# Optimization experiments

Measured on AMD Instinct MI355X. Metric: run time of the kernel, lower is better.

Reference implementation:

```python
import jax, jax.numpy as jnp
import numpy as np

jax.config.update("jax_enable_x64", True)

N = 100000          # occupied voxels
C = 64              # channels
K = 27              # 3x3x3 kernel volume
GRID = 80           # voxel grid extent
SHARED_FXP_SHIFT = 23
SHIFT0 = 31         # SharedFxpShift + requant_shift for input requant
SHIFT1 = 31         # SharedFxpShift + requant_shift after conv1+PReLU
PRELU_SHIFT = 25    # PReLU slope fixed-point shift (slope = round(a * 2^25))
ACT_RANGE = 127


def _build_neighbor_maps(rng):
    # sample N unique occupied voxels in an 80^3 grid
    flat = rng.choice(GRID ** 3, size=N, replace=False)
    x = flat // (GRID * GRID)
    y = (flat // GRID) % GRID
    z = flat % GRID
    G2 = GRID + 2  # pad by 1 so shifted coords stay in-range
    lut = -np.ones(G2 * G2 * G2, dtype=np.int64)
    lut[(x + 1) * G2 * G2 + (y + 1) * G2 + (z + 1)] = np.arange(N)
    offs = [(dx, dy, dz) for dx in (-1, 0, 1) for dy in (-1, 0, 1) for dz in (-1, 0, 1)]
    in_idx = np.empty((N, K), dtype=np.int64)
    for k, (dx, dy, dz) in enumerate(offs):
        in_idx[:, k] = lut[(x + dx + 1) * G2 * G2 + (y + dy + 1) * G2 + (z + dz + 1)]
    mask = in_idx >= 0
    in_idx = np.where(mask, in_idx, 0)
    return in_idx.astype(np.int32), mask


def setup_inputs() -> dict:
    rng = np.random.default_rng(0)
    in_idx, mask = _build_neighbor_maps(rng)
    x32 = rng.integers(-20000, 20000, size=(N, C)).astype(np.int32)
    w1 = rng.integers(-127, 128, size=(K, C, C)).astype(np.int8)   # [k, out, in]
    w2 = rng.integers(-127, 128, size=(K, C, C)).astype(np.int8)
    b1 = rng.integers(-1000, 1000, size=(C,)).astype(np.int32)
    b2 = rng.integers(-1000, 1000, size=(C,)).astype(np.int32)
    comp1 = rng.integers(-500, 500, size=(K, C)).astype(np.int32)  # zero-point compensation
    comp2 = rng.integers(-500, 500, size=(K, C)).astype(np.int32)
    mul1 = rng.integers(1000000, 1200000, size=(C,)).astype(np.int64)  # per-channel requant_mul (uint32 range)
    return {
        "x32": jnp.asarray(x32),
        "in_idx": jnp.asarray(in_idx),
        "mask": jnp.asarray(mask),
        "w1": jnp.asarray(w1), "b1": jnp.asarray(b1), "comp1": jnp.asarray(comp1),
        "w2": jnp.asarray(w2), "b2": jnp.asarray(b2), "comp2": jnp.asarray(comp2),
        "mul0": jnp.asarray(13675000, dtype=jnp.int64),
        "mul1": jnp.asarray(mul1),
        "slope": jnp.asarray(6710886, dtype=jnp.int64),  # round(0.2 * 2^25)
    }


def _requant_to_int8(x, mul, total_shift):
    # RequantFxpToScaledInt8: fixed-point multiply, arithmetic shift, clip to int8 range
    v = (x.astype(jnp.int64) * mul) >> total_shift
    return jnp.clip(v, -ACT_RANGE, ACT_RANGE).astype(jnp.int8)


def _sparse_conv_in8w8out32(f8, w, b, comp, in_idx, mask):
    # per-offset gather-GEMM-scatter, expressed as one masked gather + batched int8 GEMM
    g = jnp.where(mask[:, :, None], f8[in_idx], jnp.int8(0))           # [N, K, Cin] int8
    acc = jnp.einsum("nki,koi->no", g, w, preferred_element_type=jnp.int32)  # int32 accum
    # zero-point compensation added once per valid (offset, out) pair, plus bias
    acc = acc + mask.astype(jnp.int32) @ comp + b[None, :]
    return acc


def _prelu_int32(x, slope):
    x64 = x.astype(jnp.int64)
    return jnp.where(x64 >= 0, x64, (x64 * slope) >> PRELU_SHIFT)


def reference(x32, in_idx, mask, w1, b1, comp1, w2, b2, comp2, mul0, mul1, slope):
    q0 = _requant_to_int8(x32, mul0, SHIFT0)                 # int32 -> int8
    a1 = _sparse_conv_in8w8out32(q0, w1, b1, comp1, in_idx, mask)  # int32
    p1 = _prelu_int32(a1, slope)                             # int64 fixed-point PReLU
    q1 = _requant_to_int8(p1, mul1[None, :], SHIFT1)         # per-channel requant -> int8
    a2 = _sparse_conv_in8w8out32(q1, w2, b2, comp2, in_idx, mask)  # int32
    return a2 + x32                                          # int32 residual add
```

## Files before the change

### kernel.cpp

```cpp
#include <hip/hip_runtime.h>
#include <stdint.h>

#define CCH 64
#define KK 27
#define WN (KK * CCH * CCH)

typedef int v4i __attribute__((ext_vector_type(4)));

__global__ void __launch_bounds__(256) k_prep(
    const int* __restrict__ x32, const int* __restrict__ mul0p,
    const int* __restrict__ w1_32, const int* __restrict__ w2_32,
    const int* __restrict__ comp1, const int* __restrict__ b1,
    const int* __restrict__ comp2, const int* __restrict__ b2,
    const int* __restrict__ mask,
    int8_t* __restrict__ w1e, int8_t* __restrict__ w2e,
    int* __restrict__ q0, int* __restrict__ q1, int8_t* __restrict__ af,
    int pb1, int af_blocks, int nvox, int total4)
{
    const int bid = blockIdx.x;
    if (bid < pb1) {
        const int gtid = bid * 256 + threadIdx.x;
        if (gtid < WN) {
            w1e[gtid] = (int8_t)w1_32[gtid];
        } else if (gtid < 2 * WN) {
            w2e[gtid - WN] = (int8_t)w2_32[gtid - WN];
        } else if (gtid < 2 * WN + 8192) {
            int u = gtid - 2 * WN;
            const int which = u >> 12;
            u &= 4095;
            const int col = u >> 6, j = u & 63;
            const int* comp = which ? comp2 : comp1;
            const int* bias = which ? b2 : b1;
            int v;
            if (j < 27)       v = comp[j * CCH + col] >> 2;
            else if (j < 54)  v = comp[(j - 27) * CCH + col] & 3;
            else if (j == 54) v = bias[col] >> 6;
            else if (j == 55) v = bias[col] & 63;
            else              v = 0;
            (which ? w2e : w1e)[27 * 4096 + col * 64 + j] = (int8_t)v;
        } else {
            const int u = gtid - 2 * WN - 8192;
            if (u < 16)       q0[(size_t)nvox * 16 + u] = 0;
            else if (u < 32)  q1[(size_t)nvox * 16 + (u - 16)] = 0;
        }
    } else if (bid < pb1 + af_blocks) {
        const int vox = (bid - pb1) * 256 + threadIdx.x;
        if (vox < nvox) {
            int m[27];
#pragma unroll
            for (int k = 0; k < 27; ++k)
                m[k] = mask[(size_t)vox * 27 + k] ? 1 : 0;
            v4i d0, d1, d2, d3;
#pragma unroll
            for (int di = 0; di < 16; ++di) {
                int pk = 0;
#pragma unroll
                for (int b = 0; b < 4; ++b) {
                    const int ch = di * 4 + b;
                    int bv = 0;
                    if (ch < 27)       bv = m[ch] << 2;
                    else if (ch < 54)  bv = m[ch - 27];
                    else if (ch == 54) bv = 64;
                    else if (ch == 55) bv = 1;
                    pk |= bv << (8 * b);
                }
                if (di < 4)       d0[di] = pk;
                else if (di < 8)  d1[di - 4] = pk;
                else if (di < 12) d2[di - 8] = pk;
                else              d3[di - 12] = pk;
            }
            v4i* dst = (v4i*)(af + (size_t)vox * 64);
            dst[0] = d0; dst[1] = d1; dst[2] = d2; dst[3] = d3;
        }
    } else {
        const int i = (bid - pb1 - af_blocks) * 256 + threadIdx.x;
        if (i < total4) {
            const int mul2 = (*mul0p) << 1;
            const int4 v = ((const int4*)x32)[i];
            int r = 0, q;
            q = __mulhi(v.x, mul2); q = q > 127 ? 127 : (q < -127 ? -127 : q); r |= (q & 0xff);
            q = __mulhi(v.y, mul2); q = q > 127 ? 127 : (q < -127 ? -127 : q); r |= (q & 0xff) << 8;
            q = __mulhi(v.z, mul2); q = q > 127 ? 127 : (q < -127 ? -127 : q); r |= (q & 0xff) << 16;
            q = __mulhi(v.w, mul2); q = q > 127 ? 127 : (q < -127 ? -127 : q); r |= (q & 0xff) << 24;
            q0[i] = r;
        }
    }
}

template <int LAYER>
__global__ void __launch_bounds__(256, 2)
k_conv(const int8_t* __restrict__ fin,
       const int* __restrict__ in_idx,
       const int* __restrict__ mask,
       const int8_t* __restrict__ wext,
       const int8_t* __restrict__ af,
       const int* __restrict__ mul1,
       const int* __restrict__ slopep,
       const int* __restrict__ x32,
       int8_t* __restrict__ q1out,
       int* __restrict__ out,
       int nvox, int ntiles)
{
    __shared__ int s_off[2][16 * KK];
    __shared__ v4i s_red[2][4][4][64];

    const int tid  = threadIdx.x;
    const int lane = tid & 63;
    const int wv   = tid >> 6;
    const int arow = lane & 15;
    const int srow = lane >> 4;
    const int col  = wv * 16 + arow;
    const int e0 = tid;
    const int e1 = tid + 176;

    v4i wreg[7][4];
#pragma unroll
    for (int j = 0; j < 7; ++j)
#pragma unroll
        for (int g = 0; g < 4; ++g)
            wreg[j][g] = *(const v4i*)(wext +
                ((size_t)((7 * wv + j) * CCH + g * 16 + arow)) * CCH + srow * 16);

    const int mul2     = (LAYER == 1) ? (mul1[col] << 1) : 0;
    const int slope128 = (LAYER == 1) ? ((*slopep) << 7) : 0;

    const int stride = gridDim.x;
    const int t0 = blockIdx.x;
    if (t0 >= ntiles) return;
    const int cnt = (ntiles - 1 - t0) / stride + 1;

    v4i aA[7], aB[7];
    v4i accP = {0, 0, 0, 0};

#define GATHER_A(AN, SN, NB)                                                   \
    _Pragma("unroll")                                                          \
    for (int j = 0; j < 7; ++j) {                                              \
        if (wv == 3 && j == 6) {                                               \
            AN[6] = *(const v4i*)(af + (size_t)((NB) + arow) * CCH + srow * 16); \
        } else {                                                               \
            const int off_ = s_off[SN][arow * KK + (7 * wv + j)];              \
            AN[j] = *(const v4i*)(fin + off_ + srow * 16);                     \
        }                                                                      \
    }

#define EPILOGUE(TOT, NBP, X0, X1, X2, X3)                                     \
    if (LAYER == 1) {                                                          \
        int8_t* rp_ = q1out + (size_t)((NBP) + srow * 4) * CCH + col;          \
        _Pragma("unroll")                                                      \
        for (int r = 0; r < 4; ++r) {                                          \
            const int v_ = TOT[r];                                             \
            const int p_ = (v_ >= 0) ? v_ : __mulhi(v_, slope128);             \
            int q_ = __mulhi(p_, mul2);                                        \
            q_ = q_ > 127 ? 127 : (q_ < -127 ? -127 : q_);                     \
            rp_[r * CCH] = (int8_t)q_;                                         \
        }                                                                      \
    } else {                                                                   \
        int* rp_ = out + (size_t)((NBP) + srow * 4) * CCH + col;               \
        rp_[0 * CCH] = TOT[0] + X0;                                            \
        rp_[1 * CCH] = TOT[1] + X1;                                            \
        rp_[2 * CCH] = TOT[2] + X2;                                            \
        rp_[3 * CCH] = TOT[3] + X3;                                            \
    }

#define ITER(AC, AN, P, DO_EPI)                                                \
    do {                                                                       \
                      \
        int tp2_ = t + 2 * stride; if (tp2_ >= ntiles) tp2_ = ntiles - 1;      \
        const size_t b2_ = (size_t)tp2_ * (16 * KK);                           \
        const int qa0_ = in_idx[b2_ + e0], qm0_ = mask[b2_ + e0];              \
        const int qa1_ = in_idx[b2_ + e1], qm1_ = mask[b2_ + e1];              \
        const int nbp_ = (t - stride) * 16;                                    \
        int xr0_ = 0, xr1_ = 0, xr2_ = 0, xr3_ = 0;                            \
        if (DO_EPI && LAYER == 2) {                                            \
            const int* xp_ = x32 + (size_t)(nbp_ + srow * 4) * CCH + col;      \
            xr0_ = xp_[0 * CCH]; xr1_ = xp_[1 * CCH];                          \
            xr2_ = xp_[2 * CCH]; xr3_ = xp_[3 * CCH];                          \
        }                                                                      \
                                          \
        GATHER_A(AN, (P) ^ 1, (t + stride < ntiles ? (t + stride) * 16 : (ntiles - 1) * 16)) \
        __builtin_amdgcn_sched_barrier(0);                                     \
                                                       \
        v4i acc0 = {0,0,0,0}, acc1 = {0,0,0,0}, acc2 = {0,0,0,0}, acc3 = {0,0,0,0}; \
        _Pragma("unroll")                                                      \
        for (int j = 0; j < 7; ++j) {                                          \
            acc0 = __builtin_amdgcn_mfma_i32_16x16x64_i8(AC[j], wreg[j][0], acc0, 0, 0, 0); \
            acc1 = __builtin_amdgcn_mfma_i32_16x16x64_i8(AC[j], wreg[j][1], acc1, 0, 0, 0); \
            acc2 = __builtin_amdgcn_mfma_i32_16x16x64_i8(AC[j], wreg[j][2], acc2, 0, 0, 0); \
            acc3 = __builtin_amdgcn_mfma_i32_16x16x64_i8(AC[j], wreg[j][3], acc3, 0, 0, 0); \
        }                                                                      \
                      \
        if (wv != 0) s_red[P][wv][0][lane] = acc0;                             \
        if (wv != 1) s_red[P][wv][1][lane] = acc1;                             \
        if (wv != 2) s_red[P][wv][2][lane] = acc2;                             \
        if (wv != 3) s_red[P][wv][3][lane] = acc3;                             \
                       \
        if (DO_EPI) {                                                          \
            v4i tot = accP;                                                    \
            _Pragma("unroll")                                                  \
            for (int w = 0; w < 4; ++w) {                                      \
                if (w != wv) {                                                 \
                    const v4i r_ = s_red[(P) ^ 1][w][wv][lane];                \
                    tot[0] += r_[0]; tot[1] += r_[1];                          \
                    tot[2] += r_[2]; tot[3] += r_[3];                          \
                }                                                              \
            }                                                                  \
            EPILOGUE(tot, nbp_, xr0_, xr1_, xr2_, xr3_)                        \
        }                                                                      \
                         \
        s_off[P][e0] = (qm0_ ? qa0_ : nvox) << 6;                              \
        s_off[P][e1] = (qm1_ ? qa1_ : nvox) << 6;                              \
        accP = (wv == 0) ? acc0 : (wv == 1) ? acc1 : (wv == 2) ? acc2 : acc3;  \
        asm volatile("s_waitcnt lgkmcnt(0)" ::: "memory");                     \
        __builtin_amdgcn_s_barrier();                                          \
    } while (0)

    int pa0, pa1, pm0, pm1;
    {
        const size_t base = (size_t)t0 * (16 * KK);
        const int a0 = in_idx[base + e0], m0 = mask[base + e0];
        const int a1 = in_idx[base + e1], m1 = mask[base + e1];
        s_off[0][e0] = (m0 ? a0 : nvox) << 6;
        s_off[0][e1] = (m1 ? a1 : nvox) << 6;
    }
    {
        int t1c = t0 + stride; if (t1c >= ntiles) t1c = ntiles - 1;
        const size_t base = (size_t)t1c * (16 * KK);
        pa0 = in_idx[base + e0]; pm0 = mask[base + e0];
        pa1 = in_idx[base + e1]; pm1 = mask[base + e1];
    }
    __syncthreads();
    GATHER_A(aA, 0, t0 * 16)
    s_off[1][e0] = (pm0 ? pa0 : nvox) << 6;
    s_off[1][e1] = (pm1 ? pa1 : nvox) << 6;
    asm volatile("s_waitcnt lgkmcnt(0)" ::: "memory");
    __builtin_amdgcn_s_barrier();

    int t = t0;
    ITER(aA, aB, 0, 0);
    t += stride;
    int i = 1;
    while (i < cnt) {
        ITER(aB, aA, 1, 1);
        ++i; t += stride; if (i >= cnt) break;
        ITER(aA, aB, 0, 1);
        ++i; t += stride;
    }

    {
        const int pl = (cnt - 1) & 1;
        const int nbl = (t0 + (cnt - 1) * stride) * 16;
        int x0 = 0, x1 = 0, x2 = 0, x3 = 0;
        if (LAYER == 2) {
            const int* xp_ = x32 + (size_t)(nbl + srow * 4) * CCH + col;
            x0 = xp_[0 * CCH]; x1 = xp_[1 * CCH];
            x2 = xp_[2 * CCH]; x3 = xp_[3 * CCH];
        }
        v4i tot = accP;
#pragma unroll
        for (int w = 0; w < 4; ++w) {
            if (w != wv) {
                const v4i r_ = s_red[pl][w][wv][lane];
                tot[0] += r_[0]; tot[1] += r_[1];
                tot[2] += r_[2]; tot[3] += r_[3];
            }
        }
        EPILOGUE(tot, nbl, x0, x1, x2, x3)
    }
#undef ITER
#undef EPILOGUE
#undef GATHER_A
}

extern "C" void kernel_launch(void* const* d_in, const int* in_sizes, int n_in,
                              void* d_out, int out_size, void* d_ws, size_t ws_size,
                              hipStream_t stream) {
    const int* x32    = (const int*)d_in[0];
    const int* in_idx = (const int*)d_in[1];
    const int* mask   = (const int*)d_in[2];
    const int* w1_32  = (const int*)d_in[3];
    const int* b1     = (const int*)d_in[4];
    const int* comp1  = (const int*)d_in[5];
    const int* w2_32  = (const int*)d_in[6];
    const int* b2     = (const int*)d_in[7];
    const int* comp2  = (const int*)d_in[8];
    const int* mul0   = (const int*)d_in[9];
    const int* mul1   = (const int*)d_in[10];
    const int* slope  = (const int*)d_in[11];

    const int nvox = in_sizes[0] / CCH;
    const size_t wext_b = (size_t)28 * CCH * CCH;
    const size_t fbytes = (size_t)(nvox + 1) * CCH;
    const size_t falign = (fbytes + 255) & ~(size_t)255;
    const size_t walign = (wext_b + 255) & ~(size_t)255;

    int8_t* q0;
    int8_t* q1;
    int8_t* w1e;
    int8_t* w2e;
    int8_t* af;
    if (ws_size >= 3 * falign + 2 * walign) {
        q0  = (int8_t*)d_ws;
        q1  = q0 + falign;
        w1e = q1 + falign;
        w2e = w1e + walign;
        af  = w2e + walign;
    } else {
        q0  = (int8_t*)d_out;
        q1  = (int8_t*)d_ws;
        w1e = q1 + falign;
        w2e = w1e + walign;
        af  = w2e + walign;
    }

    const int total4 = (nvox * CCH) / 4;
    const int pb1 = (2 * WN + 8192 + 32 + 255) / 256;
    const int af_blocks  = (nvox + 255) / 256;
    const int req_blocks = (total4 + 255) / 256;
    k_prep<<<pb1 + af_blocks + req_blocks, 256, 0, stream>>>(
        x32, mul0, w1_32, w2_32, comp1, b1, comp2, b2, mask,
        w1e, w2e, (int*)q0, (int*)q1, af, pb1, af_blocks, nvox, total4);

    const int ntiles = nvox / 16;
    int cblocks = 512;
    if (cblocks > ntiles) cblocks = ntiles;
    k_conv<1><<<cblocks, 256, 0, stream>>>(q0, in_idx, mask, w1e, af,
                                           mul1, slope, nullptr,
                                           q1, nullptr, nvox, ntiles);
    k_conv<2><<<cblocks, 256, 0, stream>>>(q1, in_idx, mask, w2e, af,
                                           nullptr, nullptr, x32,
                                           nullptr, (int*)d_out, nvox, ntiles);
}
```

Measured before the change: 56.27 us.

## Fuse prep and both sparse conv layers into one cooperative persistent kernel

```diff
diff --git a/kernel.cpp b/kernel.cpp
--- a/kernel.cpp
+++ b/kernel.cpp
@@ -1,117 +1,46 @@
 #include <hip/hip_runtime.h>
+#include <hip/hip_cooperative_groups.h>
 #include <stdint.h>
+
+namespace cg = cooperative_groups;
 
 #define CCH 64
 #define KK 27
 #define WN (KK * CCH * CCH)
+#define WEXT (28 * CCH * CCH)
 
 typedef int v4i __attribute__((ext_vector_type(4)));
 
-__global__ void __launch_bounds__(256) k_prep(
-    const int* __restrict__ x32, const int* __restrict__ mul0p,
-    const int* __restrict__ w1_32, const int* __restrict__ w2_32,
-    const int* __restrict__ comp1, const int* __restrict__ b1,
-    const int* __restrict__ comp2, const int* __restrict__ b2,
-    const int* __restrict__ mask,
-    int8_t* __restrict__ w1e, int8_t* __restrict__ w2e,
-    int* __restrict__ q0, int* __restrict__ q1, int8_t* __restrict__ af,
-    int pb1, int af_blocks, int nvox, int total4)
+struct ConvShared {
+    int off[2][16][36];
+    v4i red[2][4][4][64];
+};
+
+template <int LAYER>
+__device__ void conv_phase(
+    ConvShared& sh,
+    const int8_t* __restrict__ fin, const int* __restrict__ in_idx,
+    const int* __restrict__ mask, const int8_t* __restrict__ wext,
+    const int8_t* __restrict__ af, const int* __restrict__ mul1,
+    const int* __restrict__ slopep, const int* __restrict__ x32,
+    int8_t* __restrict__ q1out, int* __restrict__ out,
+    int nvox, int ntiles)
 {
-    const int bid = blockIdx.x;
-    if (bid < pb1) {
-        const int gtid = bid * 256 + threadIdx.x;
-        if (gtid < WN) {
-            w1e[gtid] = (int8_t)w1_32[gtid];
-        } else if (gtid < 2 * WN) {
-            w2e[gtid - WN] = (int8_t)w2_32[gtid - WN];
-        } else if (gtid < 2 * WN + 8192) {
-            int u = gtid - 2 * WN;
-            const int which = u >> 12;
-            u &= 4095;
-            const int col = u >> 6, j = u & 63;
-            const int* comp = which ? comp2 : comp1;
-            const int* bias = which ? b2 : b1;
-            int v;
-            if (j < 27)       v = comp[j * CCH + col] >> 2;
-            else if (j < 54)  v = comp[(j - 27) * CCH + col] & 3;
-            else if (j == 54) v = bias[col] >> 6;
-            else if (j == 55) v = bias[col] & 63;
-            else              v = 0;
-            (which ? w2e : w1e)[27 * 4096 + col * 64 + j] = (int8_t)v;
-        } else {
-            const int u = gtid - 2 * WN - 8192;
-            if (u < 16)       q0[(size_t)nvox * 16 + u] = 0;
-            else if (u < 32)  q1[(size_t)nvox * 16 + (u - 16)] = 0;
-        }
-    } else if (bid < pb1 + af_blocks) {
-        const int vox = (bid - pb1) * 256 + threadIdx.x;
-        if (vox < nvox) {
-            int m[27];
-#pragma unroll
-            for (int k = 0; k < 27; ++k)
-                m[k] = mask[(size_t)vox * 27 + k] ? 1 : 0;
-            v4i d0, d1, d2, d3;
-#pragma unroll
-            for (int di = 0; di < 16; ++di) {
-                int pk = 0;
-#pragma unroll
-                for (int b = 0; b < 4; ++b) {
-                    const int ch = di * 4 + b;
-                    int bv = 0;
-                    if (ch < 27)       bv = m[ch] << 2;
-                    else if (ch < 54)  bv = m[ch - 27];
-                    else if (ch == 54) bv = 64;
-                    else if (ch == 55) bv = 1;
-                    pk |= bv << (8 * b);
-                }
-                if (di < 4)       d0[di] = pk;
-                else if (di < 8)  d1[di - 4] = pk;
-                else if (di < 12) d2[di - 8] = pk;
-                else              d3[di - 12] = pk;
-            }
-            v4i* dst = (v4i*)(af + (size_t)vox * 64);
-            dst[0] = d0; dst[1] = d1; dst[2] = d2; dst[3] = d3;
-        }
-    } else {
-        const int i = (bid - pb1 - af_blocks) * 256 + threadIdx.x;
-        if (i < total4) {
-            const int mul2 = (*mul0p) << 1;
-            const int4 v = ((const int4*)x32)[i];
-            int r = 0, q;
-            q = __mulhi(v.x, mul2); q = q > 127 ? 127 : (q < -127 ? -127 : q); r |= (q & 0xff);
-            q = __mulhi(v.y, mul2); q = q > 127 ? 127 : (q < -127 ? -127 : q); r |= (q & 0xff) << 8;
-            q = __mulhi(v.z, mul2); q = q > 127 ? 127 : (q < -127 ? -127 : q); r |= (q & 0xff) << 16;
-            q = __mulhi(v.w, mul2); q = q > 127 ? 127 : (q < -127 ? -127 : q); r |= (q & 0xff) << 24;
-            q0[i] = r;
-        }
-    }
-}
-
-template <int LAYER>
-__global__ void __launch_bounds__(256, 2)
-k_conv(const int8_t* __restrict__ fin,
-       const int* __restrict__ in_idx,
-       const int* __restrict__ mask,
-       const int8_t* __restrict__ wext,
-       const int8_t* __restrict__ af,
-       const int* __restrict__ mul1,
-       const int* __restrict__ slopep,
-       const int* __restrict__ x32,
-       int8_t* __restrict__ q1out,
-       int* __restrict__ out,
-       int nvox, int ntiles)
-{
-    __shared__ int s_off[2][16 * KK];
-    __shared__ v4i s_red[2][4][4][64];
-
     const int tid  = threadIdx.x;
     const int lane = tid & 63;
     const int wv   = tid >> 6;
     const int arow = lane & 15;
     const int srow = lane >> 4;
     const int col  = wv * 16 + arow;
+
     const int e0 = tid;
     const int e1 = tid + 176;
+    const int r0 = e0 / 27, s0 = e0 - r0 * 27;
+    const int r1 = e1 / 27, s1 = e1 - r1 * 27;
+    const int slot0 = r0 * 36 + (s0 / 7) * 8 + (s0 % 7);
+    const int slot1 = r1 * 36 + (s1 / 7) * 8 + (s1 % 7);
+    int* const offl = &sh.off[0][0][0];
+    const int OFFSTR = 16 * 36;
 
     v4i wreg[7][4];
 #pragma unroll
@@ -126,20 +55,24 @@
 
     const int stride = gridDim.x;
     const int t0 = blockIdx.x;
-    if (t0 >= ntiles) return;
     const int cnt = (ntiles - 1 - t0) / stride + 1;
 
     v4i aA[7], aB[7];
     v4i accP = {0, 0, 0, 0};
 
 #define GATHER_A(AN, SN, NB)                                                   \
-    _Pragma("unroll")                                                          \
-    for (int j = 0; j < 7; ++j) {                                              \
-        if (wv == 3 && j == 6) {                                               \
-            AN[6] = *(const v4i*)(af + (size_t)((NB) + arow) * CCH + srow * 16); \
-        } else {                                                               \
-            const int off_ = s_off[SN][arow * KK + (7 * wv + j)];              \
-            AN[j] = *(const v4i*)(fin + off_ + srow * 16);                     \
+    {                                                                          \
+        const v4i o0_ = *(const v4i*)&sh.off[SN][arow][wv * 8];                \
+        const v4i o1_ = *(const v4i*)&sh.off[SN][arow][wv * 8 + 4];            \
+        const int offs_[7] = {o0_[0], o0_[1], o0_[2], o0_[3],                  \
+                              o1_[0], o1_[1], o1_[2]};                         \
+        _Pragma("unroll")                                                      \
+        for (int j = 0; j < 7; ++j) {                                          \
+            if (wv == 3 && j == 6) {                                           \
+                AN[6] = *(const v4i*)(af + (size_t)((NB) + arow) * CCH + srow * 16); \
+            } else {                                                           \
+                AN[j] = *(const v4i*)(fin + offs_[j] + srow * 16);             \
+            }                                                                  \
         }                                                                      \
     }
 
@@ -164,7 +97,6 @@
 
 #define ITER(AC, AN, P, DO_EPI)                                                \
     do {                                                                       \
-                      \
         int tp2_ = t + 2 * stride; if (tp2_ >= ntiles) tp2_ = ntiles - 1;      \
         const size_t b2_ = (size_t)tp2_ * (16 * KK);                           \
         const int qa0_ = in_idx[b2_ + e0], qm0_ = mask[b2_ + e0];              \
@@ -176,11 +108,10 @@
             xr0_ = xp_[0 * CCH]; xr1_ = xp_[1 * CCH];                          \
             xr2_ = xp_[2 * CCH]; xr3_ = xp_[3 * CCH];                          \
         }                                                                      \
-                                          \
         GATHER_A(AN, (P) ^ 1, (t + stride < ntiles ? (t + stride) * 16 : (ntiles - 1) * 16)) \
         __builtin_amdgcn_sched_barrier(0);                                     \
-                                                       \
         v4i acc0 = {0,0,0,0}, acc1 = {0,0,0,0}, acc2 = {0,0,0,0}, acc3 = {0,0,0,0}; \
+        __builtin_amdgcn_s_setprio(1);                                         \
         _Pragma("unroll")                                                      \
         for (int j = 0; j < 7; ++j) {                                          \
             acc0 = __builtin_amdgcn_mfma_i32_16x16x64_i8(AC[j], wreg[j][0], acc0, 0, 0, 0); \
@@ -188,27 +119,25 @@
             acc2 = __builtin_amdgcn_mfma_i32_16x16x64_i8(AC[j], wreg[j][2], acc2, 0, 0, 0); \
             acc3 = __builtin_amdgcn_mfma_i32_16x16x64_i8(AC[j], wreg[j][3], acc3, 0, 0, 0); \
         }                                                                      \
-                      \
-        if (wv != 0) s_red[P][wv][0][lane] = acc0;                             \
-        if (wv != 1) s_red[P][wv][1][lane] = acc1;                             \
-        if (wv != 2) s_red[P][wv][2][lane] = acc2;                             \
-        if (wv != 3) s_red[P][wv][3][lane] = acc3;                             \
-                       \
+        __builtin_amdgcn_s_setprio(0);                                         \
+        if (wv != 0) sh.red[P][wv][0][lane] = acc0;                            \
+        if (wv != 1) sh.red[P][wv][1][lane] = acc1;                            \
+        if (wv != 2) sh.red[P][wv][2][lane] = acc2;                            \
+        if (wv != 3) sh.red[P][wv][3][lane] = acc3;                            \
         if (DO_EPI) {                                                          \
             v4i tot = accP;                                                    \
             _Pragma("unroll")                                                  \
             for (int w = 0; w < 4; ++w) {                                      \
                 if (w != wv) {                                                 \
-                    const v4i r_ = s_red[(P) ^ 1][w][wv][lane];                \
+                    const v4i r_ = sh.red[(P) ^ 1][w][wv][lane];               \
                     tot[0] += r_[0]; tot[1] += r_[1];                          \
                     tot[2] += r_[2]; tot[3] += r_[3];                          \
                 }                                                              \
             }                                                                  \
             EPILOGUE(tot, nbp_, xr0_, xr1_, xr2_, xr3_)                        \
         }                                                                      \
-                         \
-        s_off[P][e0] = (qm0_ ? qa0_ : nvox) << 6;                              \
-        s_off[P][e1] = (qm1_ ? qa1_ : nvox) << 6;                              \
+        offl[(P) * OFFSTR + slot0] = (qm0_ ? qa0_ : nvox) << 6;                \
+        offl[(P) * OFFSTR + slot1] = (qm1_ ? qa1_ : nvox) << 6;                \
         accP = (wv == 0) ? acc0 : (wv == 1) ? acc1 : (wv == 2) ? acc2 : acc3;  \
         asm volatile("s_waitcnt lgkmcnt(0)" ::: "memory");                     \
         __builtin_amdgcn_s_barrier();                                          \
@@ -219,8 +148,8 @@
         const size_t base = (size_t)t0 * (16 * KK);
         const int a0 = in_idx[base + e0], m0 = mask[base + e0];
         const int a1 = in_idx[base + e1], m1 = mask[base + e1];
-        s_off[0][e0] = (m0 ? a0 : nvox) << 6;
-        s_off[0][e1] = (m1 ? a1 : nvox) << 6;
+        offl[0 * OFFSTR + slot0] = (m0 ? a0 : nvox) << 6;
+        offl[0 * OFFSTR + slot1] = (m1 ? a1 : nvox) << 6;
     }
     {
         int t1c = t0 + stride; if (t1c >= ntiles) t1c = ntiles - 1;
@@ -230,8 +159,8 @@
     }
     __syncthreads();
     GATHER_A(aA, 0, t0 * 16)
-    s_off[1][e0] = (pm0 ? pa0 : nvox) << 6;
-    s_off[1][e1] = (pm1 ? pa1 : nvox) << 6;
+    offl[1 * OFFSTR + slot0] = (pm0 ? pa0 : nvox) << 6;
+    offl[1 * OFFSTR + slot1] = (pm1 ? pa1 : nvox) << 6;
     asm volatile("s_waitcnt lgkmcnt(0)" ::: "memory");
     __builtin_amdgcn_s_barrier();
 
@@ -259,7 +188,7 @@
 #pragma unroll
         for (int w = 0; w < 4; ++w) {
             if (w != wv) {
-                const v4i r_ = s_red[pl][w][wv][lane];
+                const v4i r_ = sh.red[pl][w][wv][lane];
                 tot[0] += r_[0]; tot[1] += r_[1];
                 tot[2] += r_[2]; tot[3] += r_[3];
             }
@@ -269,6 +198,89 @@
 #undef ITER
 #undef EPILOGUE
 #undef GATHER_A
+}
+
+__global__ void __launch_bounds__(256, 2) k_fused(
+    const int* x32, const int* in_idx, const int* mask,
+    const int* w1_32, const int* b1, const int* comp1,
+    const int* w2_32, const int* b2, const int* comp2,
+    const int* mul0p, const int* mul1, const int* slopep,
+    int8_t* q0, int8_t* q1, int8_t* w1e, int8_t* w2e, int8_t* af,
+    int* outp, int nvox, int ntiles, int total4)
+{
+    __shared__ ConvShared sh;
+    const int gsz = gridDim.x * 256;
+    const int g   = blockIdx.x * 256 + threadIdx.x;
+
+    for (int u = g; u < 2 * WEXT; u += gsz) {
+        const int which = u >= WEXT;
+        const int v_ = which ? u - WEXT : u;
+        int val;
+        if (v_ < WN) {
+            val = (which ? w2_32 : w1_32)[v_];
+        } else {
+            const int u2 = v_ - WN;
+            const int colx = u2 >> 6, j = u2 & 63;
+            const int* comp = which ? comp2 : comp1;
+            const int* bias = which ? b2 : b1;
+            if (j < 27)       val = comp[j * CCH + colx] >> 2;
+            else if (j < 54)  val = comp[(j - 27) * CCH + colx] & 3;
+            else if (j == 54) val = bias[colx] >> 6;
+            else if (j == 55) val = bias[colx] & 63;
+            else              val = 0;
+        }
+        (which ? w2e : w1e)[v_] = (int8_t)val;
+    }
+    for (int vox = g; vox < nvox; vox += gsz) {
+        int m[27];
+#pragma unroll
+        for (int k = 0; k < 27; ++k)
+            m[k] = mask[(size_t)vox * 27 + k] ? 1 : 0;
+        v4i d[4];
+#pragma unroll
+        for (int di = 0; di < 16; ++di) {
+            int pk = 0;
+#pragma unroll
+            for (int b = 0; b < 4; ++b) {
+                const int ch = di * 4 + b;
+                int bv = 0;
+                if (ch < 27)       bv = m[ch] << 2;
+                else if (ch < 54)  bv = m[ch - 27];
+                else if (ch == 54) bv = 64;
+                else if (ch == 55) bv = 1;
+                pk |= bv << (8 * b);
+            }
+            d[di >> 2][di & 3] = pk;
+        }
+        v4i* dst = (v4i*)(af + (size_t)vox * 64);
+        dst[0] = d[0]; dst[1] = d[1]; dst[2] = d[2]; dst[3] = d[3];
+    }
+    {
+        const int mul2 = (*mul0p) << 1;
+        for (int i = g; i < total4; i += gsz) {
+            const int4 v = ((const int4*)x32)[i];
+            int r = 0, q;
+            q = __mulhi(v.x, mul2); q = q > 127 ? 127 : (q < -127 ? -127 : q); r |= (q & 0xff);
+            q = __mulhi(v.y, mul2); q = q > 127 ? 127 : (q < -127 ? -127 : q); r |= (q & 0xff) << 8;
+            q = __mulhi(v.z, mul2); q = q > 127 ? 127 : (q < -127 ? -127 : q); r |= (q & 0xff) << 16;
+            q = __mulhi(v.w, mul2); q = q > 127 ? 127 : (q < -127 ? -127 : q); r |= (q & 0xff) << 24;
+            ((int*)q0)[i] = r;
+        }
+    }
+    if (g < 16)      ((int*)q0)[(size_t)nvox * 16 + g] = 0;
+    else if (g < 32) ((int*)q1)[(size_t)nvox * 16 + (g - 16)] = 0;
+
+    __threadfence();
+    cg::this_grid().sync();
+
+    conv_phase<1>(sh, q0, in_idx, mask, w1e, af, mul1, slopep,
+                  nullptr, q1, nullptr, nvox, ntiles);
+
+    __threadfence();
+    cg::this_grid().sync();
+
+    conv_phase<2>(sh, q1, in_idx, mask, w2e, af, nullptr, nullptr,
+                  x32, nullptr, outp, nvox, ntiles);
 }
 
 extern "C" void kernel_launch(void* const* d_in, const int* in_sizes, int n_in,
@@ -288,10 +300,9 @@
     const int* slope  = (const int*)d_in[11];
 
     const int nvox = in_sizes[0] / CCH;
-    const size_t wext_b = (size_t)28 * CCH * CCH;
     const size_t fbytes = (size_t)(nvox + 1) * CCH;
     const size_t falign = (fbytes + 255) & ~(size_t)255;
-    const size_t walign = (wext_b + 255) & ~(size_t)255;
+    const size_t walign = ((size_t)WEXT + 255) & ~(size_t)255;
 
     int8_t* q0;
     int8_t* q1;
@@ -312,21 +323,26 @@
         af  = w2e + walign;
     }
 
-    const int total4 = (nvox * CCH) / 4;
-    const int pb1 = (2 * WN + 8192 + 32 + 255) / 256;
-    const int af_blocks  = (nvox + 255) / 256;
-    const int req_blocks = (total4 + 255) / 256;
-    k_prep<<<pb1 + af_blocks + req_blocks, 256, 0, stream>>>(
-        x32, mul0, w1_32, w2_32, comp1, b1, comp2, b2, mask,
-        w1e, w2e, (int*)q0, (int*)q1, af, pb1, af_blocks, nvox, total4);
-
-    const int ntiles = nvox / 16;
-    int cblocks = 512;
-    if (cblocks > ntiles) cblocks = ntiles;
-    k_conv<1><<<cblocks, 256, 0, stream>>>(q0, in_idx, mask, w1e, af,
-                                           mul1, slope, nullptr,
-                                           q1, nullptr, nvox, ntiles);
-    k_conv<2><<<cblocks, 256, 0, stream>>>(q1, in_idx, mask, w2e, af,
-                                           nullptr, nullptr, x32,
-                                           nullptr, (int*)d_out, nvox, ntiles);
+    int ntiles = nvox / 16;
+    int total4 = nvox * 16;
+    int* outp  = (int*)d_out;
+
+    int maxb = 0;
+    (void)hipOccupancyMaxActiveBlocksPerMultiprocessor(
+        &maxb, reinterpret_cast<const void*>(k_fused), 256, 0);
+    if (maxb < 1) maxb = 1;
+    int grid = maxb * 256;
+    if (grid > 512) grid = 512;
+    if (grid > ntiles) grid = ntiles;
+
+    void* args[] = {
+        (void*)&x32, (void*)&in_idx, (void*)&mask,
+        (void*)&w1_32, (void*)&b1, (void*)&comp1,
+        (void*)&w2_32, (void*)&b2, (void*)&comp2,
+        (void*)&mul0, (void*)&mul1, (void*)&slope,
+        (void*)&q0, (void*)&q1, (void*)&w1e, (void*)&w2e, (void*)&af,
+        (void*)&outp, (void*)&nvox, (void*)&ntiles, (void*)&total4
+    };
+    hipLaunchCooperativeKernel(reinterpret_cast<void*>(k_fused),
+                               dim3(grid), dim3(256), args, 0, stream);
 }
```

Measured after the change: 197.2 us. 250% more time.
